# Optimization experiments

Measured on AMD Instinct MI355X. Metric: run time of the kernel, lower is better.

The kernel has to match this reference:

```python
import jax, jax.numpy as jnp
import numpy as np

JITTER = 0.002  # original adds 0.001*I globally plus 0.001*I on each diagonal block


def setup_inputs() -> dict:
    key = jax.random.key(0)
    k1, k2, k3 = jax.random.split(key, 3)
    T, N, D, Z = 4, 1024, 64, 4
    x = jax.random.normal(k1, (T, N, D), dtype=jnp.float32)      # per-task features
    W = jax.random.normal(k2, (T, Z), dtype=jnp.float32)         # task-to-latent mixing weights
    theta = jax.random.uniform(k3, (Z, 2), dtype=jnp.float32)    # [amplitude, inv-lengthscale] per latent GP
    return {"x": x, "W": W, "theta": theta}


def reference(x, W, theta):
    # Faithful, fused version of MTGP.rbf_kernel_mo_hete with x2=None and equal
    # task lengths. cov[mi, nj] = sum_z W[task(mi),z] W[task(nj),z] * theta[z,0]
    #   * exp(-theta[z,1]/2 * ||X[mi]-X[nj]||^2)  + JITTER on the diagonal.
    T, N, D = x.shape
    Z = theta.shape[0]
    M = T * N
    X = x.reshape(M, D)
    sq = jnp.sum(X * X, axis=-1)                                  # [M]
    sqd = jnp.maximum(sq[:, None] + sq[None, :] - 2.0 * X @ X.T, 0.0)  # [M, M]
    Wexp = jnp.repeat(W, N, axis=0)                               # [M, Z] task weight per point
    cov = JITTER * jnp.eye(M, dtype=x.dtype)
    for z in range(Z):  # small fixed loop over latent GPs
        Kz = theta[z, 0] * jnp.exp(-0.5 * theta[z, 1] * sqd)      # [M, M]
        cov = cov + (Wexp[:, z][:, None] * Wexp[:, z][None, :]) * Kz
    return cov
```

## Files before the change

### kernel.cpp

```cpp
#include <hip/hip_runtime.h>


#define M_PTS 4096
#define DIM 64
#define JITTER_F 0.002f
#define NEG_HALF_LOG2E (-0.72134752044448170f)
#define NBLK 2080

typedef __attribute__((ext_vector_type(8))) short short8v;
typedef __attribute__((ext_vector_type(4))) float f32x4;

union FragU { short8v v; uint4 u; };

__device__ __forceinline__ float fast_exp2(float x) {
#if defined(__has_builtin)
#if __has_builtin(__builtin_amdgcn_exp2f)
  return __builtin_amdgcn_exp2f(x);
#else
  return exp2f(x);
#endif
#else
  return exp2f(x);
#endif
}

__device__ __forceinline__ unsigned bfr(float x) {
  unsigned u = __float_as_uint(x);
  return (u + 0x7FFFu + ((u >> 16) & 1u)) >> 16;
}
__device__ __forceinline__ float bff(unsigned h) {
  return __uint_as_float(h << 16);
}

__global__ __launch_bounds__(256, 5) void mtgp_fused(
    const float* __restrict__ X,
    const float* __restrict__ W,
    const float* __restrict__ theta,
    float* __restrict__ out) {
  __shared__ unsigned short Ahi[64 * 64], Alo[64 * 64];
  __shared__ unsigned short Bhi[64 * 64], Blo[64 * 64];

  const int item = blockIdx.x;
  int u = (int)(64.5f - sqrtf(4160.25f - 2.0f * (float)item));
  if (u < 0) u = 0;
  if (u > 63) u = 63;
  while (u > 0 && u * (129 - u) / 2 > item) --u;
  while (u < 63 && (u + 1) * (128 - u) / 2 <= item) ++u;
  const int v = u + (item - u * (129 - u) / 2);
  const int grow0 = u << 6, gj0 = v << 6;

  const int tid = threadIdx.x;

  const int half = tid & 1;
  const int srow = (tid & 127) >> 1;
  const bool isB = (tid >= 128);
  const int gsrow = (isB ? gj0 : grow0) + srow;
  const float4* xr = (const float4*)(X + (size_t)gsrow * DIM + half * 32);
  unsigned short* Ph = isB ? Bhi : Ahi;
  unsigned short* Pl = isB ? Blo : Alo;
  float s = 0.0f;
#pragma unroll
  for (int kgs = 0; kgs < 4; ++kgs) {
    const float4 v0 = xr[kgs];
    const float4 v1 = xr[kgs + 4];
    s = fmaf(v0.x, v0.x, s); s = fmaf(v0.y, v0.y, s);
    s = fmaf(v0.z, v0.z, s); s = fmaf(v0.w, v0.w, s);
    s = fmaf(v1.x, v1.x, s); s = fmaf(v1.y, v1.y, s);
    s = fmaf(v1.z, v1.z, s); s = fmaf(v1.w, v1.w, s);
    const unsigned h0 = bfr(v0.x), h1 = bfr(v0.y), h2 = bfr(v0.z), h3 = bfr(v0.w);
    const unsigned h4 = bfr(v1.x), h5 = bfr(v1.y), h6 = bfr(v1.z), h7 = bfr(v1.w);
    uint4 hv = make_uint4(h0 | (h1 << 16), h2 | (h3 << 16),
                          h4 | (h5 << 16), h6 | (h7 << 16));
    const unsigned l0 = bfr(v0.x - bff(h0)), l1 = bfr(v0.y - bff(h1));
    const unsigned l2 = bfr(v0.z - bff(h2)), l3 = bfr(v0.w - bff(h3));
    const unsigned l4 = bfr(v1.x - bff(h4)), l5 = bfr(v1.y - bff(h5));
    const unsigned l6 = bfr(v1.z - bff(h6)), l7 = bfr(v1.w - bff(h7));
    uint4 lv = make_uint4(l0 | (l1 << 16), l2 | (l3 << 16),
                          l4 | (l5 << 16), l6 | (l7 << 16));
    const int f = (half << 2) + kgs;
    const int lofs = srow * 64 + ((f ^ (srow & 7)) << 3);
    *(uint4*)&Ph[lofs] = hv;
    *(uint4*)&Pl[lofs] = lv;
  }
  s += __shfl_xor(s, 1);
  __syncthreads();

  const int wid = tid >> 6, lane = tid & 63;
  const int wr = (wid >> 1) << 5;
  const int wc = (wid & 1) << 5;
  const int r16 = lane & 15, kg = lane >> 4, kg4 = kg << 2;

  f32x4 acc[2][2];
#pragma unroll
  for (int p = 0; p < 2; ++p) { acc[p][0] = (f32x4)0.0f; acc[p][1] = (f32x4)0.0f; }

#define FRAG_LD(dst, PANEL, rr) { \
    dst.u = *(const uint4*)&PANEL[(rr) * 64 + ((f0 ^ ((rr) & 7)) << 3)]; }

#pragma unroll
  for (int k0 = 0; k0 < 2; ++k0) {
    const int f0 = (k0 << 2) + kg;
    FragU ah[2], al[2], bh[2], bl[2];
#pragma unroll
    for (int p = 0; p < 2; ++p) {
      const int ra = wr + p * 16 + r16;
      const int rb = wc + p * 16 + r16;
      FRAG_LD(ah[p], Ahi, ra)
      FRAG_LD(al[p], Alo, ra)
      FRAG_LD(bh[p], Bhi, rb)
      FRAG_LD(bl[p], Blo, rb)
    }
#pragma unroll
    for (int p = 0; p < 2; ++p)
#pragma unroll
      for (int q = 0; q < 2; ++q) {
        acc[p][q] = __builtin_amdgcn_mfma_f32_16x16x32_bf16(ah[p].v, bh[q].v, acc[p][q], 0, 0, 0);
        acc[p][q] = __builtin_amdgcn_mfma_f32_16x16x32_bf16(ah[p].v, bl[q].v, acc[p][q], 0, 0, 0);
        acc[p][q] = __builtin_amdgcn_mfma_f32_16x16x32_bf16(al[p].v, bh[q].v, acc[p][q], 0, 0, 0);
      }
  }
#undef FRAG_LD

  __syncthreads();
  if (half == 0) ((float*)Ahi)[(isB ? 64 : 0) + srow] = s;
  __syncthreads();
  const float* nrm = (const float*)Ahi;

  const int ti = u >> 4, tj = v >> 4;
  float czv[4], ezv[4];
#pragma unroll
  for (int z = 0; z < 4; ++z) {
    czv[z] = W[ti * 4 + z] * W[tj * 4 + z] * theta[2 * z];
    ezv[z] = NEG_HALF_LOG2E * theta[2 * z + 1];
  }
  f32x4 sqr[2];
#pragma unroll
  for (int p = 0; p < 2; ++p) sqr[p] = *(const f32x4*)&nrm[wr + p * 16 + kg4];
  float sqc[2];
#pragma unroll
  for (int q = 0; q < 2; ++q) sqc[q] = nrm[64 + wc + q * 16 + r16];

#pragma unroll
  for (int p = 0; p < 2; ++p)
#pragma unroll
    for (int q = 0; q < 2; ++q)
#pragma unroll
      for (int rr = 0; rr < 4; ++rr) {
        const float d = acc[p][q][rr];
        const float sd = fmaxf(fmaf(-2.0f, d, sqr[p][rr] + sqc[q]), 0.0f);
        float val = czv[0] * fast_exp2(ezv[0] * sd);
        val = fmaf(czv[1], fast_exp2(ezv[1] * sd), val);
        val = fmaf(czv[2], fast_exp2(ezv[2] * sd), val);
        val = fmaf(czv[3], fast_exp2(ezv[3] * sd), val);
        if (u == v && wr + p * 16 + kg4 + rr == wc + q * 16 + r16) val += JITTER_F;
        acc[p][q][rr] = val;
      }

#pragma unroll
  for (int p = 0; p < 2; ++p)
#pragma unroll
    for (int rr = 0; rr < 4; ++rr) {
      float* rp = out + (size_t)(grow0 + wr + p * 16 + kg4 + rr) * M_PTS + gj0 + wc + r16;
      rp[0] = acc[p][0][rr];
      rp[16] = acc[p][1][rr];
    }
  if (u != v) {
#pragma unroll
    for (int q = 0; q < 2; ++q)
#pragma unroll
      for (int p = 0; p < 2; ++p) {
        f32x4* tp = (f32x4*)(out + (size_t)(gj0 + wc + q * 16 + r16) * M_PTS + grow0 + wr + p * 16 + kg4);
        *tp = acc[p][q];
      }
  }
}

extern "C" void kernel_launch(void* const* d_in, const int* in_sizes, int n_in,
                              void* d_out, int out_size, void* d_ws, size_t ws_size,
                              hipStream_t stream) {
  const float* x     = (const float*)d_in[0];
  const float* W     = (const float*)d_in[1];
  const float* theta = (const float*)d_in[2];
  float* out = (float*)d_out;

  mtgp_fused<<<dim3(NBLK), dim3(256), 0, stream>>>(x, W, theta, out);
}
```

Baseline: 24.29 us.

## Stage K in two halves to halve LDS footprint and raise occupancy

```diff
diff --git a/kernel.cpp b/kernel.cpp
--- a/kernel.cpp
+++ b/kernel.cpp
@@ -32,13 +32,17 @@
   return __uint_as_float(h << 16);
 }
 
-__global__ __launch_bounds__(256, 5) void mtgp_fused(
+__device__ __forceinline__ int poff(int row, int s) {
+  return ((row >> 1) << 6) + ((row & 1) << 5) + ((s ^ ((row >> 1) & 3)) << 3);
+}
+
+__global__ __launch_bounds__(256, 7) void mtgp_fused(
     const float* __restrict__ X,
     const float* __restrict__ W,
     const float* __restrict__ theta,
     float* __restrict__ out) {
-  __shared__ unsigned short Ahi[64 * 64], Alo[64 * 64];
-  __shared__ unsigned short Bhi[64 * 64], Blo[64 * 64];
+  __shared__ __align__(16) unsigned short Ahi[2048], Alo[2048];
+  __shared__ __align__(16) unsigned short Bhi[2048], Blo[2048];
 
   const int item = blockIdx.x;
   int u = (int)(64.5f - sqrtf(4160.25f - 2.0f * (float)item));
@@ -50,41 +54,7 @@
   const int grow0 = u << 6, gj0 = v << 6;
 
   const int tid = threadIdx.x;
-
-  const int half = tid & 1;
-  const int srow = (tid & 127) >> 1;
-  const bool isB = (tid >= 128);
-  const int gsrow = (isB ? gj0 : grow0) + srow;
-  const float4* xr = (const float4*)(X + (size_t)gsrow * DIM + half * 32);
-  unsigned short* Ph = isB ? Bhi : Ahi;
-  unsigned short* Pl = isB ? Blo : Alo;
-  float s = 0.0f;
-#pragma unroll
-  for (int kgs = 0; kgs < 4; ++kgs) {
-    const float4 v0 = xr[kgs];
-    const float4 v1 = xr[kgs + 4];
-    s = fmaf(v0.x, v0.x, s); s = fmaf(v0.y, v0.y, s);
-    s = fmaf(v0.z, v0.z, s); s = fmaf(v0.w, v0.w, s);
-    s = fmaf(v1.x, v1.x, s); s = fmaf(v1.y, v1.y, s);
-    s = fmaf(v1.z, v1.z, s); s = fmaf(v1.w, v1.w, s);
-    const unsigned h0 = bfr(v0.x), h1 = bfr(v0.y), h2 = bfr(v0.z), h3 = bfr(v0.w);
-    const unsigned h4 = bfr(v1.x), h5 = bfr(v1.y), h6 = bfr(v1.z), h7 = bfr(v1.w);
-    uint4 hv = make_uint4(h0 | (h1 << 16), h2 | (h3 << 16),
-                          h4 | (h5 << 16), h6 | (h7 << 16));
-    const unsigned l0 = bfr(v0.x - bff(h0)), l1 = bfr(v0.y - bff(h1));
-    const unsigned l2 = bfr(v0.z - bff(h2)), l3 = bfr(v0.w - bff(h3));
-    const unsigned l4 = bfr(v1.x - bff(h4)), l5 = bfr(v1.y - bff(h5));
-    const unsigned l6 = bfr(v1.z - bff(h6)), l7 = bfr(v1.w - bff(h7));
-    uint4 lv = make_uint4(l0 | (l1 << 16), l2 | (l3 << 16),
-                          l4 | (l5 << 16), l6 | (l7 << 16));
-    const int f = (half << 2) + kgs;
-    const int lofs = srow * 64 + ((f ^ (srow & 7)) << 3);
-    *(uint4*)&Ph[lofs] = hv;
-    *(uint4*)&Pl[lofs] = lv;
-  }
-  s += __shfl_xor(s, 1);
-  __syncthreads();
-
+  const int srow = tid >> 2, seg = tid & 3;
   const int wid = tid >> 6, lane = tid & 63;
   const int wr = (wid >> 1) << 5;
   const int wc = (wid & 1) << 5;
@@ -94,35 +64,78 @@
 #pragma unroll
   for (int p = 0; p < 2; ++p) { acc[p][0] = (f32x4)0.0f; acc[p][1] = (f32x4)0.0f; }
 
-#define FRAG_LD(dst, PANEL, rr) { \
-    dst.u = *(const uint4*)&PANEL[(rr) * 64 + ((f0 ^ ((rr) & 7)) << 3)]; }
-
-#pragma unroll
+  float sA = 0.0f, sB = 0.0f;
+  const int lofs = poff(srow, seg);
+
+#pragma unroll 1
   for (int k0 = 0; k0 < 2; ++k0) {
-    const int f0 = (k0 << 2) + kg;
-    FragU ah[2], al[2], bh[2], bl[2];
-#pragma unroll
-    for (int p = 0; p < 2; ++p) {
-      const int ra = wr + p * 16 + r16;
-      const int rb = wc + p * 16 + r16;
-      FRAG_LD(ah[p], Ahi, ra)
-      FRAG_LD(al[p], Alo, ra)
-      FRAG_LD(bh[p], Bhi, rb)
-      FRAG_LD(bl[p], Blo, rb)
+    {
+      const float* pa = X + (size_t)(grow0 + srow) * DIM + k0 * 32 + seg * 8;
+      const float* pb = X + (size_t)(gj0 + srow) * DIM + k0 * 32 + seg * 8;
+      const float4 a0 = *(const float4*)pa, a1 = *(const float4*)(pa + 4);
+      const float4 b0 = *(const float4*)pb, b1 = *(const float4*)(pb + 4);
+      sA = fmaf(a0.x, a0.x, sA); sA = fmaf(a0.y, a0.y, sA);
+      sA = fmaf(a0.z, a0.z, sA); sA = fmaf(a0.w, a0.w, sA);
+      sA = fmaf(a1.x, a1.x, sA); sA = fmaf(a1.y, a1.y, sA);
+      sA = fmaf(a1.z, a1.z, sA); sA = fmaf(a1.w, a1.w, sA);
+      sB = fmaf(b0.x, b0.x, sB); sB = fmaf(b0.y, b0.y, sB);
+      sB = fmaf(b0.z, b0.z, sB); sB = fmaf(b0.w, b0.w, sB);
+      sB = fmaf(b1.x, b1.x, sB); sB = fmaf(b1.y, b1.y, sB);
+      sB = fmaf(b1.z, b1.z, sB); sB = fmaf(b1.w, b1.w, sB);
+      const unsigned h0 = bfr(a0.x), h1 = bfr(a0.y), h2 = bfr(a0.z), h3 = bfr(a0.w);
+      const unsigned h4 = bfr(a1.x), h5 = bfr(a1.y), h6 = bfr(a1.z), h7 = bfr(a1.w);
+      const uint4 ahv = make_uint4(h0 | (h1 << 16), h2 | (h3 << 16),
+                                   h4 | (h5 << 16), h6 | (h7 << 16));
+      const uint4 alv = make_uint4(
+          bfr(a0.x - bff(h0)) | (bfr(a0.y - bff(h1)) << 16),
+          bfr(a0.z - bff(h2)) | (bfr(a0.w - bff(h3)) << 16),
+          bfr(a1.x - bff(h4)) | (bfr(a1.y - bff(h5)) << 16),
+          bfr(a1.z - bff(h6)) | (bfr(a1.w - bff(h7)) << 16));
+      const unsigned g0 = bfr(b0.x), g1 = bfr(b0.y), g2 = bfr(b0.z), g3 = bfr(b0.w);
+      const unsigned g4 = bfr(b1.x), g5 = bfr(b1.y), g6 = bfr(b1.z), g7 = bfr(b1.w);
+      const uint4 bhv = make_uint4(g0 | (g1 << 16), g2 | (g3 << 16),
+                                   g4 | (g5 << 16), g6 | (g7 << 16));
+      const uint4 blv = make_uint4(
+          bfr(b0.x - bff(g0)) | (bfr(b0.y - bff(g1)) << 16),
+          bfr(b0.z - bff(g2)) | (bfr(b0.w - bff(g3)) << 16),
+          bfr(b1.x - bff(g4)) | (bfr(b1.y - bff(g5)) << 16),
+          bfr(b1.z - bff(g6)) | (bfr(b1.w - bff(g7)) << 16));
+      *(uint4*)&Ahi[lofs] = ahv;
+      *(uint4*)&Alo[lofs] = alv;
+      *(uint4*)&Bhi[lofs] = bhv;
+      *(uint4*)&Blo[lofs] = blv;
     }
-#pragma unroll
-    for (int p = 0; p < 2; ++p)
-#pragma unroll
-      for (int q = 0; q < 2; ++q) {
-        acc[p][q] = __builtin_amdgcn_mfma_f32_16x16x32_bf16(ah[p].v, bh[q].v, acc[p][q], 0, 0, 0);
-        acc[p][q] = __builtin_amdgcn_mfma_f32_16x16x32_bf16(ah[p].v, bl[q].v, acc[p][q], 0, 0, 0);
-        acc[p][q] = __builtin_amdgcn_mfma_f32_16x16x32_bf16(al[p].v, bh[q].v, acc[p][q], 0, 0, 0);
+    __syncthreads();
+
+    {
+      FragU ah[2], al[2], bh[2], bl[2];
+#pragma unroll
+      for (int p = 0; p < 2; ++p) {
+        const int ra = wr + p * 16 + r16;
+        const int rb = wc + p * 16 + r16;
+        ah[p].u = *(const uint4*)&Ahi[poff(ra, kg)];
+        al[p].u = *(const uint4*)&Alo[poff(ra, kg)];
+        bh[p].u = *(const uint4*)&Bhi[poff(rb, kg)];
+        bl[p].u = *(const uint4*)&Blo[poff(rb, kg)];
       }
-  }
-#undef FRAG_LD
-
-  __syncthreads();
-  if (half == 0) ((float*)Ahi)[(isB ? 64 : 0) + srow] = s;
+#pragma unroll
+      for (int p = 0; p < 2; ++p)
+#pragma unroll
+        for (int q = 0; q < 2; ++q) {
+          acc[p][q] = __builtin_amdgcn_mfma_f32_16x16x32_bf16(ah[p].v, bh[q].v, acc[p][q], 0, 0, 0);
+          acc[p][q] = __builtin_amdgcn_mfma_f32_16x16x32_bf16(ah[p].v, bl[q].v, acc[p][q], 0, 0, 0);
+          acc[p][q] = __builtin_amdgcn_mfma_f32_16x16x32_bf16(al[p].v, bh[q].v, acc[p][q], 0, 0, 0);
+        }
+    }
+    __syncthreads();
+  }
+
+  sA += __shfl_xor(sA, 1); sA += __shfl_xor(sA, 2);
+  sB += __shfl_xor(sB, 1); sB += __shfl_xor(sB, 2);
+  if (seg == 0) {
+    ((float*)Ahi)[srow] = sA;
+    ((float*)Ahi)[64 + srow] = sB;
+  }
   __syncthreads();
   const float* nrm = (const float*)Ahi;
 
```

Result: slower. 25.29 us (+4.1%).

## Make tile kernel persistent with prefetch of next tile's panels

Applied to the files above, without the earlier changes.

```diff
diff --git a/kernel.cpp b/kernel.cpp
--- a/kernel.cpp
+++ b/kernel.cpp
@@ -5,7 +5,6 @@
 #define DIM 64
 #define JITTER_F 0.002f
 #define NEG_HALF_LOG2E (-0.72134752044448170f)
-#define NBLK 2080
 
 typedef __attribute__((ext_vector_type(8))) short short8v;
 typedef __attribute__((ext_vector_type(4))) float f32x4;
@@ -32,146 +31,195 @@
   return __uint_as_float(h << 16);
 }
 
-__global__ __launch_bounds__(256, 5) void mtgp_fused(
-    const float* __restrict__ X,
-    const float* __restrict__ W,
-    const float* __restrict__ theta,
-    float* __restrict__ out) {
-  __shared__ unsigned short Ahi[64 * 64], Alo[64 * 64];
-  __shared__ unsigned short Bhi[64 * 64], Blo[64 * 64];
-
-  const int item = blockIdx.x;
-  int u = (int)(64.5f - sqrtf(4160.25f - 2.0f * (float)item));
-  if (u < 0) u = 0;
-  if (u > 63) u = 63;
-  while (u > 0 && u * (129 - u) / 2 > item) --u;
-  while (u < 63 && (u + 1) * (128 - u) / 2 <= item) ++u;
-  const int v = u + (item - u * (129 - u) / 2);
-  const int grow0 = u << 6, gj0 = v << 6;
-
-  const int tid = threadIdx.x;
-
-  const int half = tid & 1;
-  const int srow = (tid & 127) >> 1;
-  const bool isB = (tid >= 128);
-  const int gsrow = (isB ? gj0 : grow0) + srow;
-  const float4* xr = (const float4*)(X + (size_t)gsrow * DIM + half * 32);
-  unsigned short* Ph = isB ? Bhi : Ahi;
-  unsigned short* Pl = isB ? Blo : Alo;
+__device__ __forceinline__ void cvt_write(const float4* xv, unsigned short* Ph,
+                                          unsigned short* Pl, int srow, int half,
+                                          float& sout) {
   float s = 0.0f;
 #pragma unroll
   for (int kgs = 0; kgs < 4; ++kgs) {
-    const float4 v0 = xr[kgs];
-    const float4 v1 = xr[kgs + 4];
+    const float4 v0 = xv[kgs];
+    const float4 v1 = xv[kgs + 4];
     s = fmaf(v0.x, v0.x, s); s = fmaf(v0.y, v0.y, s);
     s = fmaf(v0.z, v0.z, s); s = fmaf(v0.w, v0.w, s);
     s = fmaf(v1.x, v1.x, s); s = fmaf(v1.y, v1.y, s);
     s = fmaf(v1.z, v1.z, s); s = fmaf(v1.w, v1.w, s);
     const unsigned h0 = bfr(v0.x), h1 = bfr(v0.y), h2 = bfr(v0.z), h3 = bfr(v0.w);
     const unsigned h4 = bfr(v1.x), h5 = bfr(v1.y), h6 = bfr(v1.z), h7 = bfr(v1.w);
-    uint4 hv = make_uint4(h0 | (h1 << 16), h2 | (h3 << 16),
-                          h4 | (h5 << 16), h6 | (h7 << 16));
-    const unsigned l0 = bfr(v0.x - bff(h0)), l1 = bfr(v0.y - bff(h1));
-    const unsigned l2 = bfr(v0.z - bff(h2)), l3 = bfr(v0.w - bff(h3));
-    const unsigned l4 = bfr(v1.x - bff(h4)), l5 = bfr(v1.y - bff(h5));
-    const unsigned l6 = bfr(v1.z - bff(h6)), l7 = bfr(v1.w - bff(h7));
-    uint4 lv = make_uint4(l0 | (l1 << 16), l2 | (l3 << 16),
-                          l4 | (l5 << 16), l6 | (l7 << 16));
+    const uint4 hv = make_uint4(h0 | (h1 << 16), h2 | (h3 << 16),
+                                h4 | (h5 << 16), h6 | (h7 << 16));
+    const uint4 lv = make_uint4(
+        bfr(v0.x - bff(h0)) | (bfr(v0.y - bff(h1)) << 16),
+        bfr(v0.z - bff(h2)) | (bfr(v0.w - bff(h3)) << 16),
+        bfr(v1.x - bff(h4)) | (bfr(v1.y - bff(h5)) << 16),
+        bfr(v1.z - bff(h6)) | (bfr(v1.w - bff(h7)) << 16));
     const int f = (half << 2) + kgs;
     const int lofs = srow * 64 + ((f ^ (srow & 7)) << 3);
     *(uint4*)&Ph[lofs] = hv;
     *(uint4*)&Pl[lofs] = lv;
   }
-  s += __shfl_xor(s, 1);
-  __syncthreads();
-
+  sout = s;
+}
+
+__device__ __forceinline__ void decode_item(int item, int& uu, int& vv) {
+  int u = (int)(64.5f - sqrtf(4160.25f - 2.0f * (float)item));
+  if (u < 0) u = 0;
+  if (u > 63) u = 63;
+  while (u > 0 && u * (129 - u) / 2 > item) --u;
+  while (u < 63 && (u + 1) * (128 - u) / 2 <= item) ++u;
+  uu = u;
+  vv = u + (item - u * (129 - u) / 2);
+}
+
+__global__ __launch_bounds__(256, 4) void mtgp_persist(
+    const float* __restrict__ X,
+    const float* __restrict__ W,
+    const float* __restrict__ theta,
+    float* __restrict__ out) {
+  __shared__ __align__(16) unsigned short Ahi[4096], Alo[4096];
+  __shared__ __align__(16) unsigned short Bhi[4096], Blo[4096];
+  __shared__ float nrm[2][128];
+
+  const int b = blockIdx.x;
+  const int nt = (b < 32) ? 3 : 2;
+
+  const int tid = threadIdx.x;
+  const int half = tid & 1;
+  const int srow = (tid & 127) >> 1;
+  const bool isB = (tid >= 128);
   const int wid = tid >> 6, lane = tid & 63;
   const int wr = (wid >> 1) << 5;
   const int wc = (wid & 1) << 5;
   const int r16 = lane & 15, kg = lane >> 4, kg4 = kg << 2;
 
-  f32x4 acc[2][2];
-#pragma unroll
-  for (int p = 0; p < 2; ++p) { acc[p][0] = (f32x4)0.0f; acc[p][1] = (f32x4)0.0f; }
-
+  int u, v;
+  decode_item(2 * b, u, v);
+  int curU = u;
+
+  {
+    float4 xv[8];
+    const int grow = ((isB ? v : u) << 6) + srow;
+    const float4* xr = (const float4*)(X + (size_t)grow * DIM + half * 32);
+#pragma unroll
+    for (int i = 0; i < 8; ++i) xv[i] = xr[i];
+    float s;
+    cvt_write(xv, isB ? Bhi : Ahi, isB ? Blo : Alo, srow, half, s);
+    s += __shfl_xor(s, 1);
+    if (half == 0) nrm[0][(isB ? 64 : 0) + srow] = s;
+  }
+  __syncthreads();
+
+#pragma unroll 1
+  for (int t = 0; t < nt; ++t) {
+    const int bank = t & 1;
+    const int grow0 = u << 6, gj0 = v << 6;
+
+    f32x4 acc[2][2];
+#pragma unroll
+    for (int p = 0; p < 2; ++p) { acc[p][0] = (f32x4)0.0f; acc[p][1] = (f32x4)0.0f; }
 #define FRAG_LD(dst, PANEL, rr) { \
     dst.u = *(const uint4*)&PANEL[(rr) * 64 + ((f0 ^ ((rr) & 7)) << 3)]; }
-
-#pragma unroll
-  for (int k0 = 0; k0 < 2; ++k0) {
-    const int f0 = (k0 << 2) + kg;
-    FragU ah[2], al[2], bh[2], bl[2];
-#pragma unroll
-    for (int p = 0; p < 2; ++p) {
-      const int ra = wr + p * 16 + r16;
-      const int rb = wc + p * 16 + r16;
-      FRAG_LD(ah[p], Ahi, ra)
-      FRAG_LD(al[p], Alo, ra)
-      FRAG_LD(bh[p], Bhi, rb)
-      FRAG_LD(bl[p], Blo, rb)
-    }
+#pragma unroll
+    for (int k0 = 0; k0 < 2; ++k0) {
+      const int f0 = (k0 << 2) + kg;
+      FragU ah[2], al[2], bh[2], bl[2];
+#pragma unroll
+      for (int p = 0; p < 2; ++p) {
+        const int ra = wr + p * 16 + r16;
+        const int rb = wc + p * 16 + r16;
+        FRAG_LD(ah[p], Ahi, ra)
+        FRAG_LD(al[p], Alo, ra)
+        FRAG_LD(bh[p], Bhi, rb)
+        FRAG_LD(bl[p], Blo, rb)
+      }
+#pragma unroll
+      for (int p = 0; p < 2; ++p)
+#pragma unroll
+        for (int q = 0; q < 2; ++q) {
+          acc[p][q] = __builtin_amdgcn_mfma_f32_16x16x32_bf16(ah[p].v, bh[q].v, acc[p][q], 0, 0, 0);
+          acc[p][q] = __builtin_amdgcn_mfma_f32_16x16x32_bf16(ah[p].v, bl[q].v, acc[p][q], 0, 0, 0);
+          acc[p][q] = __builtin_amdgcn_mfma_f32_16x16x32_bf16(al[p].v, bh[q].v, acc[p][q], 0, 0, 0);
+        }
+    }
+#undef FRAG_LD
+    __syncthreads();
+
+    const bool hav = (t + 1 < nt);
+    int u2 = u, v2 = v;
+    bool iload = false;
+    float4 xv[8];
+    if (hav) {
+      decode_item((t + 1 == 1) ? (2 * b + 1) : (2048 + b), u2, v2);
+      const bool achg = (u2 != curU);
+      iload = isB || achg;
+      if (iload) {
+        const int grow = ((isB ? v2 : u2) << 6) + srow;
+        const float4* xr = (const float4*)(X + (size_t)grow * DIM + half * 32);
+#pragma unroll
+        for (int i = 0; i < 8; ++i) xv[i] = xr[i];
+      }
+      if (!achg && tid < 64) nrm[bank ^ 1][tid] = nrm[bank][tid];
+    }
+
+    const int ti = u >> 4, tj = v >> 4;
+    float czv[4], ezv[4];
+#pragma unroll
+    for (int z = 0; z < 4; ++z) {
+      czv[z] = W[ti * 4 + z] * W[tj * 4 + z] * theta[2 * z];
+      ezv[z] = NEG_HALF_LOG2E * theta[2 * z + 1];
+    }
+    f32x4 sqr[2];
+#pragma unroll
+    for (int p = 0; p < 2; ++p) sqr[p] = *(const f32x4*)&nrm[bank][wr + p * 16 + kg4];
+    float sqc[2];
+#pragma unroll
+    for (int q = 0; q < 2; ++q) sqc[q] = nrm[bank][64 + wc + q * 16 + r16];
+
 #pragma unroll
     for (int p = 0; p < 2; ++p)
 #pragma unroll
-      for (int q = 0; q < 2; ++q) {
-        acc[p][q] = __builtin_amdgcn_mfma_f32_16x16x32_bf16(ah[p].v, bh[q].v, acc[p][q], 0, 0, 0);
-        acc[p][q] = __builtin_amdgcn_mfma_f32_16x16x32_bf16(ah[p].v, bl[q].v, acc[p][q], 0, 0, 0);
-        acc[p][q] = __builtin_amdgcn_mfma_f32_16x16x32_bf16(al[p].v, bh[q].v, acc[p][q], 0, 0, 0);
-      }
-  }
-#undef FRAG_LD
-
-  __syncthreads();
-  if (half == 0) ((float*)Ahi)[(isB ? 64 : 0) + srow] = s;
-  __syncthreads();
-  const float* nrm = (const float*)Ahi;
-
-  const int ti = u >> 4, tj = v >> 4;
-  float czv[4], ezv[4];
-#pragma unroll
-  for (int z = 0; z < 4; ++z) {
-    czv[z] = W[ti * 4 + z] * W[tj * 4 + z] * theta[2 * z];
-    ezv[z] = NEG_HALF_LOG2E * theta[2 * z + 1];
-  }
-  f32x4 sqr[2];
-#pragma unroll
-  for (int p = 0; p < 2; ++p) sqr[p] = *(const f32x4*)&nrm[wr + p * 16 + kg4];
-  float sqc[2];
-#pragma unroll
-  for (int q = 0; q < 2; ++q) sqc[q] = nrm[64 + wc + q * 16 + r16];
-
-#pragma unroll
-  for (int p = 0; p < 2; ++p)
-#pragma unroll
-    for (int q = 0; q < 2; ++q)
+      for (int q = 0; q < 2; ++q)
+#pragma unroll
+        for (int rr = 0; rr < 4; ++rr) {
+          const float d = acc[p][q][rr];
+          const float sd = fmaxf(fmaf(-2.0f, d, sqr[p][rr] + sqc[q]), 0.0f);
+          float val = czv[0] * fast_exp2(ezv[0] * sd);
+          val = fmaf(czv[1], fast_exp2(ezv[1] * sd), val);
+          val = fmaf(czv[2], fast_exp2(ezv[2] * sd), val);
+          val = fmaf(czv[3], fast_exp2(ezv[3] * sd), val);
+          if (u == v && wr + p * 16 + kg4 + rr == wc + q * 16 + r16) val += JITTER_F;
+          acc[p][q][rr] = val;
+        }
+
+#pragma unroll
+    for (int p = 0; p < 2; ++p)
 #pragma unroll
       for (int rr = 0; rr < 4; ++rr) {
-        const float d = acc[p][q][rr];
-        const float sd = fmaxf(fmaf(-2.0f, d, sqr[p][rr] + sqc[q]), 0.0f);
-        float val = czv[0] * fast_exp2(ezv[0] * sd);
-        val = fmaf(czv[1], fast_exp2(ezv[1] * sd), val);
-        val = fmaf(czv[2], fast_exp2(ezv[2] * sd), val);
-        val = fmaf(czv[3], fast_exp2(ezv[3] * sd), val);
-        if (u == v && wr + p * 16 + kg4 + rr == wc + q * 16 + r16) val += JITTER_F;
-        acc[p][q][rr] = val;
-      }
-
-#pragma unroll
-  for (int p = 0; p < 2; ++p)
-#pragma unroll
-    for (int rr = 0; rr < 4; ++rr) {
-      float* rp = out + (size_t)(grow0 + wr + p * 16 + kg4 + rr) * M_PTS + gj0 + wc + r16;
-      rp[0] = acc[p][0][rr];
-      rp[16] = acc[p][1][rr];
-    }
-  if (u != v) {
-#pragma unroll
-    for (int q = 0; q < 2; ++q)
-#pragma unroll
-      for (int p = 0; p < 2; ++p) {
-        f32x4* tp = (f32x4*)(out + (size_t)(gj0 + wc + q * 16 + r16) * M_PTS + grow0 + wr + p * 16 + kg4);
-        *tp = acc[p][q];
-      }
+        float* rp = out + (size_t)(grow0 + wr + p * 16 + kg4 + rr) * M_PTS + gj0 + wc + r16;
+        rp[0] = acc[p][0][rr];
+        rp[16] = acc[p][1][rr];
+      }
+    if (u != v) {
+#pragma unroll
+      for (int q = 0; q < 2; ++q)
+#pragma unroll
+        for (int p = 0; p < 2; ++p) {
+          f32x4* tp = (f32x4*)(out + (size_t)(gj0 + wc + q * 16 + r16) * M_PTS + grow0 + wr + p * 16 + kg4);
+          *tp = acc[p][q];
+        }
+    }
+
+    if (hav) {
+      if (iload) {
+        float s;
+        cvt_write(xv, isB ? Bhi : Ahi, isB ? Blo : Alo, srow, half, s);
+        s += __shfl_xor(s, 1);
+        if (half == 0) nrm[bank ^ 1][(isB ? 64 : 0) + srow] = s;
+      }
+      curU = u2;
+      u = u2;
+      v = v2;
+    }
+    __syncthreads();
   }
 }
 
@@ -183,5 +231,5 @@
   const float* theta = (const float*)d_in[2];
   float* out = (float*)d_out;
 
-  mtgp_fused<<<dim3(NBLK), dim3(256), 0, stream>>>(x, W, theta, out);
-}
+  mtgp_persist<<<dim3(1024), dim3(256), 0, stream>>>(x, W, theta, out);
+}
```

Result: slower. 28.15 us (+15.9%).
